# Performance work log

Measured on AMD Instinct MI355X. Metric: run time of the kernel, lower is better.

Reference implementation:

```python
import jax, jax.numpy as jnp
import numpy as np

H, D = 4, 64  # num_heads, hidden_feats
IN_FEATS, OUT_FEATS = 1, 128
N_NODES, N_EDGES = 100000, 1600000
NEG_SLOPE = 0.2  # DGL GATConv default


def setup_inputs() -> dict:
    key = jax.random.key(0)
    ks = jax.random.split(key, 9)
    features = jax.random.normal(ks[0], (N_NODES, IN_FEATS), dtype=jnp.float32)
    src = jax.random.randint(ks[1], (N_EDGES,), 0, N_NODES)
    dst = jax.random.randint(ks[2], (N_EDGES,), 0, N_NODES)
    # GATConv params
    W = jax.random.normal(ks[3], (IN_FEATS, H * D), dtype=jnp.float32) * 0.5
    attn_l = jax.random.normal(ks[4], (H, D), dtype=jnp.float32) * 0.1
    attn_r = jax.random.normal(ks[5], (H, D), dtype=jnp.float32) * 0.1
    bias_gat = jnp.zeros((H * D,), dtype=jnp.float32)
    # fc params
    fc_W = jax.random.normal(ks[6], (H * D, OUT_FEATS), dtype=jnp.float32) * 0.05
    fc_b = jax.random.normal(ks[7], (OUT_FEATS,), dtype=jnp.float32) * 0.01
    return {"features": features, "W": W, "attn_l": attn_l, "attn_r": attn_r,
            "bias_gat": bias_gat, "fc_W": fc_W, "fc_b": fc_b,
            "src": src, "dst": dst}


def reference(features, W, attn_l, attn_r, bias_gat, fc_W, fc_b, src, dst):
    N = features.shape[0]
    # linear projection -> [N, H, D]
    feat = (features @ W).reshape(N, H, D)
    # per-node attention terms [N, H]
    el = jnp.einsum('nhd,hd->nh', feat, attn_l)
    er = jnp.einsum('nhd,hd->nh', feat, attn_r)
    # per-edge scores [E, H]
    e = jax.nn.leaky_relu(el[src] + er[dst], NEG_SLOPE)
    # segment softmax over incoming edges of each dst node
    emax = jax.ops.segment_max(e, dst, num_segments=N)  # [N, H]
    ee = jnp.exp(e - emax[dst])
    denom = jax.ops.segment_sum(ee, dst, num_segments=N)  # [N, H]
    alpha = ee / denom[dst]  # [E, H]
    # attention-weighted aggregation: scatter-add messages to dst
    msg = alpha[:, :, None] * feat[src]  # [E, H, D]
    rst = jax.ops.segment_sum(msg, dst, num_segments=N)  # [N, H, D]
    rst = rst + bias_gat.reshape(1, H, D)
    h = rst.reshape(N, H * D)
    out = h @ fc_W + fc_b  # [N, OUT_FEATS]
    return out.mean(axis=0)  # [OUT_FEATS]
```

## Files before the change

kernel.cpp:

```cpp
#include <hip/hip_runtime.h>

#define NEG_SLOPE 0.2f

#define GB_SHIFT 9
#define GB_NODES 512
#define GCAP 9216
#define NBLK 512
#define MAXB 256
#define SCHUNK 4096

#define DESC_OFF 1024
#define REC_OFF  (DESC_OFF + NBLK * MAXB * 4)


__global__ __launch_bounds__(512) void k_place(const int* __restrict__ src,
                                               const int* __restrict__ dst,
                                               int* __restrict__ desc,
                                               unsigned* __restrict__ rec,
                                               float* __restrict__ hdr,
                                               int E, int nbins, int chunk) {
    __shared__ unsigned      raw[SCHUNK];
    __shared__ unsigned char binb[SCHUNK];
    __shared__ unsigned      sorted[SCHUNK];
    __shared__ int hist[MAXB], startS[MAXB], cur[MAXB];
    __shared__ int wtot[4], wpre[4];

    int tid = threadIdx.x, blk = blockIdx.x;
    int lane = tid & 63, wave = tid >> 6;
    if (blk == 0 && tid < 16) hdr[tid] = 0.f;
    if (tid < MAXB) hist[tid] = 0;
    __syncthreads();

    int lo = blk * chunk;
    int hi = lo + chunk; if (hi > E) hi = E;
    int tot = hi - lo;

    for (int i = tid; i < tot; i += 512) {
        int d = dst[lo + i], s = src[lo + i];
        int b = d >> GB_SHIFT;
        raw[i]  = ((unsigned)(d & (GB_NODES - 1)) << 17) | (unsigned)s;
        binb[i] = (unsigned char)b;
        atomicAdd(&hist[b], 1);
    }
    __syncthreads();

    int h = 0, x = 0;
    if (tid < MAXB) {
        h = hist[tid]; x = h;
        #pragma unroll
        for (int off = 1; off < 64; off <<= 1) {
            int y = __shfl_up(x, off, 64);
            if (lane >= off) x += y;
        }
        if (lane == 63) wtot[wave] = x;
    }
    __syncthreads();
    if (tid < 4) {
        int t = wtot[tid];
        #pragma unroll
        for (int off = 1; off < 4; off <<= 1) {
            int y = __shfl_up(t, off, 64);
            if (tid >= off) t += y;
        }
        wpre[tid] = t - wtot[tid];
    }
    __syncthreads();
    if (tid < MAXB) {
        int ex = (x - h) + wpre[wave];
        startS[tid] = ex;
        cur[tid] = ex;
    }
    __syncthreads();

    for (int i = tid; i < tot; i += 512) {
        int p = atomicAdd(&cur[binb[i]], 1);
        sorted[p] = raw[i];
    }
    __syncthreads();

    size_t base = (size_t)blk * SCHUNK;
    for (int i = tid; i < tot; i += 512)
        rec[base + i] = sorted[i];
    if (tid < MAXB)
        desc[(size_t)blk * MAXB + tid] = (startS[tid] << 16) | hist[tid];
}

__global__ __launch_bounds__(512) void k_gather(const float* __restrict__ f,
                                                const float* __restrict__ W,
                                                const float* __restrict__ attn_l,
                                                const float* __restrict__ attn_r,
                                                const int* __restrict__ desc,
                                                const unsigned* __restrict__ rec,
                                                float* __restrict__ S_sum,
                                                int N) {
    __shared__ float    par[8];
    __shared__ int      deg[GB_NODES], nstart[GB_NODES], ncur[GB_NODES];
    __shared__ unsigned stageu[GCAP];
    __shared__ float    sortedf[GCAP];
    __shared__ int      wtot[8], wpre[8], cntS;
    __shared__ float    sm[8][4];

    int tid = threadIdx.x, lane = tid & 63, wave = tid >> 6;
    int bin = blockIdx.x, nbase = bin << GB_SHIFT;

    if (tid < 256) {
        float w  = W[tid];
        float vl = w * attn_l[tid];
        float vr = w * attn_r[tid];
        #pragma unroll
        for (int off = 32; off > 0; off >>= 1) {
            vl += __shfl_down(vl, off, 64);
            vr += __shfl_down(vr, off, 64);
        }
        if ((tid & 63) == 0) {
            int hh = tid >> 6;
            par[hh]     = vl;
            par[4 + hh] = vr;
        }
    }
    deg[tid] = 0;

    int dsc  = desc[(size_t)tid * MAXB + bin];
    int sst  = dsc >> 16, scnt = dsc & 0xFFFF;

    int x = scnt;
    #pragma unroll
    for (int off = 1; off < 64; off <<= 1) {
        int y = __shfl_up(x, off, 64);
        if (lane >= off) x += y;
    }
    if (lane == 63) wtot[wave] = x;
    __syncthreads();
    if (tid < 8) {
        int t = wtot[tid];
        #pragma unroll
        for (int off = 1; off < 8; off <<= 1) {
            int y = __shfl_up(t, off, 64);
            if (tid >= off) t += y;
        }
        wpre[tid] = t - wtot[tid];
        if (tid == 7) cntS = t;
    }
    __syncthreads();
    int soff = (x - scnt) + wpre[wave];

    float al[4], ar[4];
    #pragma unroll
    for (int h = 0; h < 4; ++h) { al[h] = par[h]; ar[h] = par[4 + h]; }

    {
        const unsigned* r0 = rec + (size_t)tid * SCHUNK + sst;
        for (int i = 0; i < scnt; ++i) {
            unsigned rc = r0[i];
            int p = soff + i;
            if (p < GCAP) {
                stageu[p] = rc;
                atomicAdd(&deg[rc >> 17], 1);
            }
        }
    }
    __syncthreads();
    int cnt = cntS; if (cnt > GCAP) cnt = GCAP;

    int dv = deg[tid];
    int x2 = dv;
    #pragma unroll
    for (int off = 1; off < 64; off <<= 1) {
        int y = __shfl_up(x2, off, 64);
        if (lane >= off) x2 += y;
    }
    if (lane == 63) wtot[wave] = x2;
    __syncthreads();
    if (tid < 8) {
        int t = wtot[tid];
        #pragma unroll
        for (int off = 1; off < 8; off <<= 1) {
            int y = __shfl_up(t, off, 64);
            if (tid >= off) t += y;
        }
        wpre[tid] = t - wtot[tid];
    }
    __syncthreads();
    int ex = (x2 - dv) + wpre[wave];
    nstart[tid] = ex;
    ncur[tid]   = ex;
    __syncthreads();

    for (int i = tid; i < cnt; i += 512) {
        unsigned rc = stageu[i];
        int p = atomicAdd(&ncur[rc >> 17], 1);
        if (p < GCAP) sortedf[p] = f[rc & 0x1FFFF];
    }
    __syncthreads();

    int st  = nstart[tid];
    int len = deg[tid];
    int en  = st + len; if (en > GCAP) en = GCAP; if (st > GCAP) st = GCAP;
    float fd = (len > 0) ? f[nbase + tid] : 0.f;

    float dn[4] = {0.f, 0.f, 0.f, 0.f};
    float nm[4] = {0.f, 0.f, 0.f, 0.f};
    float br[4];
    #pragma unroll
    for (int h = 0; h < 4; ++h) br[h] = fd * ar[h];
    for (int i = st; i < en; ++i) {
        float fs = sortedf[i];
        #pragma unroll
        for (int h = 0; h < 4; ++h) {
            float xx = fmaf(fs, al[h], br[h]);
            xx = (xx > 0.f) ? xx : NEG_SLOPE * xx;
            float ee = __expf(xx);
            dn[h] += ee;
            nm[h] += ee * fs;
        }
    }
    float v[4];
    #pragma unroll
    for (int h = 0; h < 4; ++h)
        v[h] = (dn[h] > 0.f) ? nm[h] / dn[h] : 0.f;

    #pragma unroll
    for (int off = 32; off > 0; off >>= 1) {
        #pragma unroll
        for (int h = 0; h < 4; ++h) v[h] += __shfl_down(v[h], off, 64);
    }
    if (lane == 0) {
        #pragma unroll
        for (int h = 0; h < 4; ++h) sm[wave][h] = v[h];
    }
    __syncthreads();
    if (tid < 4) {
        float s = 0.f;
        #pragma unroll
        for (int w = 0; w < 8; ++w) s += sm[w][tid];
        atomicAdd(&S_sum[tid], s);
    }
}


__global__ void k_prep(const float* __restrict__ W,
                       const float* __restrict__ attn_l,
                       const float* __restrict__ attn_r,
                       float* __restrict__ ws) {
    int tid = threadIdx.x;
    float w  = W[tid];
    float vl = w * attn_l[tid];
    float vr = w * attn_r[tid];
    #pragma unroll
    for (int off = 32; off > 0; off >>= 1) {
        vl += __shfl_down(vl, off, 64);
        vr += __shfl_down(vr, off, 64);
    }
    if ((tid & 63) == 0) {
        int h = tid >> 6;
        ws[h]     = vl;
        ws[4 + h] = vr;
    }
}

__global__ void k_edge(const float* __restrict__ f,
                       const int* __restrict__ src,
                       const int* __restrict__ dst,
                       const float* __restrict__ par,
                       float* __restrict__ denom,
                       float* __restrict__ numer,
                       int E) {
    float al[4], ar[4];
    #pragma unroll
    for (int h = 0; h < 4; ++h) { al[h] = par[h]; ar[h] = par[4 + h]; }
    int stride = gridDim.x * blockDim.x;
    for (int e = blockIdx.x * blockDim.x + threadIdx.x; e < E; e += stride) {
        int s = src[e], d = dst[e];
        float fs = f[s], fd = f[d];
        #pragma unroll
        for (int h = 0; h < 4; ++h) {
            float x = fs * al[h] + fd * ar[h];
            x = (x > 0.f) ? x : NEG_SLOPE * x;
            float ee = __expf(x);
            atomicAdd(&denom[d * 4 + h], ee);
            atomicAdd(&numer[d * 4 + h], ee * fs);
        }
    }
}

__global__ void k_node(const float* __restrict__ denom,
                       const float* __restrict__ numer,
                       float* __restrict__ S_sum,
                       int N) {
    float acc[4] = {0.f, 0.f, 0.f, 0.f};
    int stride = gridDim.x * blockDim.x;
    for (int n = blockIdx.x * blockDim.x + threadIdx.x; n < N; n += stride) {
        float4 dn = *reinterpret_cast<const float4*>(&denom[(size_t)n * 4]);
        float4 nm = *reinterpret_cast<const float4*>(&numer[(size_t)n * 4]);
        acc[0] += (dn.x > 0.f) ? nm.x / dn.x : 0.f;
        acc[1] += (dn.y > 0.f) ? nm.y / dn.y : 0.f;
        acc[2] += (dn.z > 0.f) ? nm.z / dn.z : 0.f;
        acc[3] += (dn.w > 0.f) ? nm.w / dn.w : 0.f;
    }
    #pragma unroll
    for (int off = 32; off > 0; off >>= 1) {
        #pragma unroll
        for (int h = 0; h < 4; ++h) acc[h] += __shfl_down(acc[h], off, 64);
    }
    __shared__ float sm[4][4];
    int lane = threadIdx.x & 63;
    int wave = threadIdx.x >> 6;
    if (lane == 0) {
        #pragma unroll
        for (int h = 0; h < 4; ++h) sm[wave][h] = acc[h];
    }
    __syncthreads();
    if (threadIdx.x < 4) {
        float v = sm[0][threadIdx.x] + sm[1][threadIdx.x]
                + sm[2][threadIdx.x] + sm[3][threadIdx.x];
        atomicAdd(&S_sum[threadIdx.x], v);
    }
}

__global__ __launch_bounds__(512) void k_final(const float* __restrict__ ws,
                                               const float* __restrict__ W,
                                               const float* __restrict__ bias_gat,
                                               const float* __restrict__ fc_W,
                                               const float* __restrict__ fc_b,
                                               float* __restrict__ out,
                                               float invN) {
    __shared__ float sm[4][128];
    int tid = threadIdx.x;
    int o = tid & 127, part = tid >> 7;
    float sp = ws[8 + part] * invN;
    float acc = 0.f;
    #pragma unroll 4
    for (int k = 0; k < 64; ++k) {
        int hd = part * 64 + k;
        float rm = sp * W[hd] + bias_gat[hd];
        acc += rm * fc_W[hd * 128 + o];
    }
    sm[part][o] = acc;
    __syncthreads();
    if (tid < 128)
        out[tid] = sm[0][tid] + sm[1][tid] + sm[2][tid] + sm[3][tid] + fc_b[tid];
}

extern "C" void kernel_launch(void* const* d_in, const int* in_sizes, int n_in,
                              void* d_out, int out_size, void* d_ws, size_t ws_size,
                              hipStream_t stream) {
    const float* features = (const float*)d_in[0];
    const float* W        = (const float*)d_in[1];
    const float* attn_l   = (const float*)d_in[2];
    const float* attn_r   = (const float*)d_in[3];
    const float* bias_gat = (const float*)d_in[4];
    const float* fc_W     = (const float*)d_in[5];
    const float* fc_b     = (const float*)d_in[6];
    const int*   src      = (const int*)d_in[7];
    const int*   dst      = (const int*)d_in[8];
    int N = in_sizes[0];
    int E = in_sizes[7];

    float* ws = (float*)d_ws;
    int nbins = (N + GB_NODES - 1) >> GB_SHIFT;
    int chunk = (E + NBLK - 1) / NBLK;
    size_t need = (size_t)REC_OFF + (size_t)NBLK * SCHUNK * sizeof(unsigned);

    if (nbins <= MAXB && N <= (1 << 17) && chunk <= SCHUNK && ws_size >= need) {
        int* desc     = (int*)((char*)d_ws + DESC_OFF);
        unsigned* rec = (unsigned*)((char*)d_ws + REC_OFF);

        hipLaunchKernelGGL(k_place, dim3(NBLK), dim3(512), 0, stream,
                           src, dst, desc, rec, ws, E, nbins, chunk);
        hipLaunchKernelGGL(k_gather, dim3(nbins), dim3(512), 0, stream,
                           features, W, attn_l, attn_r, desc, rec, ws + 8, N);
    } else {
        float* denom = ws + 16;
        float* numer = denom + (size_t)N * 4;
        size_t zero_bytes = (16 + 2 * (size_t)N * 4) * sizeof(float);
        hipMemsetAsync(d_ws, 0, zero_bytes, stream);
        hipLaunchKernelGGL(k_prep, dim3(1), dim3(256), 0, stream, W, attn_l, attn_r, ws);
        int eb = (E + 255) / 256;
        hipLaunchKernelGGL(k_edge, dim3(eb), dim3(256), 0, stream,
                           features, src, dst, ws, denom, numer, E);
        int nb = (N + 255) / 256;
        if (nb > 2048) nb = 2048;
        hipLaunchKernelGGL(k_node, dim3(nb), dim3(256), 0, stream, denom, numer, ws + 8, N);
    }

    hipLaunchKernelGGL(k_final, dim3(1), dim3(512), 0, stream,
                       ws, W, bias_gat, fc_W, fc_b, (float*)d_out, 1.0f / (float)N);
}
```

Measured before the change: 48.50 us.

## Halve gather bin size and split each node's edge loop across two threads

Destination bins shrink from 512 to 256 nodes, so the gather kernel launches about twice as many blocks, each with a smaller shared staging buffer. The place kernel now handles 512 bins, using 16-bit bin ids and a full 512-thread histogram scan. In the gather kernel, two threads share each destination node and take alternating edges, then combine their partial sums with a lane shuffle. The aim is better occupancy across the CUs and shorter serial per-node loops. In exchange, the place kernel does more scan and descriptor work, and the per-bin capacity margin is tighter.

```diff
diff --git a/kernel.cpp b/kernel.cpp
--- a/kernel.cpp
+++ b/kernel.cpp
@@ -2,11 +2,11 @@
 
 #define NEG_SLOPE 0.2f
 
-#define GB_SHIFT 9
-#define GB_NODES 512
-#define GCAP 9216
+#define GB_SHIFT 8
+#define GB_NODES 256
+#define GCAP 4864
 #define NBLK 512
-#define MAXB 256
+#define MAXB 512
 #define SCHUNK 4096
 
 #define DESC_OFF 1024
@@ -19,16 +19,16 @@
                                                unsigned* __restrict__ rec,
                                                float* __restrict__ hdr,
                                                int E, int nbins, int chunk) {
-    __shared__ unsigned      raw[SCHUNK];
-    __shared__ unsigned char binb[SCHUNK];
-    __shared__ unsigned      sorted[SCHUNK];
+    __shared__ unsigned       raw[SCHUNK];
+    __shared__ unsigned short binb[SCHUNK];
+    __shared__ unsigned       sorted[SCHUNK];
     __shared__ int hist[MAXB], startS[MAXB], cur[MAXB];
-    __shared__ int wtot[4], wpre[4];
+    __shared__ int wtot[8], wpre[8];
 
     int tid = threadIdx.x, blk = blockIdx.x;
     int lane = tid & 63, wave = tid >> 6;
     if (blk == 0 && tid < 16) hdr[tid] = 0.f;
-    if (tid < MAXB) hist[tid] = 0;
+    hist[tid] = 0;
     __syncthreads();
 
     int lo = blk * chunk;
@@ -39,37 +39,33 @@
         int d = dst[lo + i], s = src[lo + i];
         int b = d >> GB_SHIFT;
         raw[i]  = ((unsigned)(d & (GB_NODES - 1)) << 17) | (unsigned)s;
-        binb[i] = (unsigned char)b;
+        binb[i] = (unsigned short)b;
         atomicAdd(&hist[b], 1);
     }
     __syncthreads();
 
-    int h = 0, x = 0;
-    if (tid < MAXB) {
-        h = hist[tid]; x = h;
-        #pragma unroll
-        for (int off = 1; off < 64; off <<= 1) {
-            int y = __shfl_up(x, off, 64);
-            if (lane >= off) x += y;
-        }
-        if (lane == 63) wtot[wave] = x;
-    }
-    __syncthreads();
-    if (tid < 4) {
+    int h = hist[tid];
+    int x = h;
+    #pragma unroll
+    for (int off = 1; off < 64; off <<= 1) {
+        int y = __shfl_up(x, off, 64);
+        if (lane >= off) x += y;
+    }
+    if (lane == 63) wtot[wave] = x;
+    __syncthreads();
+    if (tid < 8) {
         int t = wtot[tid];
         #pragma unroll
-        for (int off = 1; off < 4; off <<= 1) {
+        for (int off = 1; off < 8; off <<= 1) {
             int y = __shfl_up(t, off, 64);
             if (tid >= off) t += y;
         }
         wpre[tid] = t - wtot[tid];
     }
     __syncthreads();
-    if (tid < MAXB) {
-        int ex = (x - h) + wpre[wave];
-        startS[tid] = ex;
-        cur[tid] = ex;
-    }
+    int ex = (x - h) + wpre[wave];
+    startS[tid] = ex;
+    cur[tid] = ex;
     __syncthreads();
 
     for (int i = tid; i < tot; i += 512) {
@@ -81,8 +77,7 @@
     size_t base = (size_t)blk * SCHUNK;
     for (int i = tid; i < tot; i += 512)
         rec[base + i] = sorted[i];
-    if (tid < MAXB)
-        desc[(size_t)blk * MAXB + tid] = (startS[tid] << 16) | hist[tid];
+    desc[(size_t)blk * MAXB + tid] = (startS[tid] << 16) | hist[tid];
 }
 
 __global__ __launch_bounds__(512) void k_gather(const float* __restrict__ f,
@@ -117,8 +112,8 @@
             par[hh]     = vl;
             par[4 + hh] = vr;
         }
-    }
-    deg[tid] = 0;
+        deg[tid] = 0;
+    }
 
     int dsc  = desc[(size_t)tid * MAXB + bin];
     int sst  = dsc >> 16, scnt = dsc & 0xFFFF;
@@ -162,28 +157,33 @@
     __syncthreads();
     int cnt = cntS; if (cnt > GCAP) cnt = GCAP;
 
-    int dv = deg[tid];
-    int x2 = dv;
-    #pragma unroll
-    for (int off = 1; off < 64; off <<= 1) {
-        int y = __shfl_up(x2, off, 64);
-        if (lane >= off) x2 += y;
-    }
-    if (lane == 63) wtot[wave] = x2;
-    __syncthreads();
-    if (tid < 8) {
-        int t = wtot[tid];
-        #pragma unroll
-        for (int off = 1; off < 8; off <<= 1) {
-            int y = __shfl_up(t, off, 64);
-            if (tid >= off) t += y;
-        }
-        wpre[tid] = t - wtot[tid];
-    }
-    __syncthreads();
-    int ex = (x2 - dv) + wpre[wave];
-    nstart[tid] = ex;
-    ncur[tid]   = ex;
+    if (tid < GB_NODES) {
+        int dv = deg[tid];
+        int x2 = dv;
+        #pragma unroll
+        for (int off = 1; off < 64; off <<= 1) {
+            int y = __shfl_up(x2, off, 64);
+            if (lane >= off) x2 += y;
+        }
+        if (lane == 63) wtot[wave] = x2;
+        __syncthreads();
+        if (tid < 4) {
+            int t = wtot[tid];
+            #pragma unroll
+            for (int off = 1; off < 4; off <<= 1) {
+                int y = __shfl_up(t, off, 64);
+                if (tid >= off) t += y;
+            }
+            wpre[tid] = t - wtot[tid];
+        }
+        __syncthreads();
+        int ex = (x2 - dv) + wpre[wave];
+        nstart[tid] = ex;
+        ncur[tid]   = ex;
+    } else {
+        __syncthreads();
+        __syncthreads();
+    }
     __syncthreads();
 
     for (int i = tid; i < cnt; i += 512) {
@@ -193,17 +193,18 @@
     }
     __syncthreads();
 
-    int st  = nstart[tid];
-    int len = deg[tid];
+    int l   = tid >> 1, prt = tid & 1;
+    int st  = nstart[l];
+    int len = deg[l];
     int en  = st + len; if (en > GCAP) en = GCAP; if (st > GCAP) st = GCAP;
-    float fd = (len > 0) ? f[nbase + tid] : 0.f;
+    float fd = (len > 0) ? f[nbase + l] : 0.f;
 
     float dn[4] = {0.f, 0.f, 0.f, 0.f};
     float nm[4] = {0.f, 0.f, 0.f, 0.f};
     float br[4];
     #pragma unroll
     for (int h = 0; h < 4; ++h) br[h] = fd * ar[h];
-    for (int i = st; i < en; ++i) {
+    for (int i = st + prt; i < en; i += 2) {
         float fs = sortedf[i];
         #pragma unroll
         for (int h = 0; h < 4; ++h) {
@@ -216,8 +217,11 @@
     }
     float v[4];
     #pragma unroll
-    for (int h = 0; h < 4; ++h)
-        v[h] = (dn[h] > 0.f) ? nm[h] / dn[h] : 0.f;
+    for (int h = 0; h < 4; ++h) {
+        dn[h] += __shfl_xor(dn[h], 1, 64);
+        nm[h] += __shfl_xor(nm[h], 1, 64);
+        v[h] = (prt == 0 && dn[h] > 0.f) ? nm[h] / dn[h] : 0.f;
+    }
 
     #pragma unroll
     for (int off = 32; off > 0; off >>= 1) {
```

After: 45.79 us. -5.6%, faster.
